# Optimization experiments

Hardware: AMD Instinct MI355X
Metric: run time of the kernel (lower is better)

## Reference

```python
import jax, jax.numpy as jnp
import numpy as np

H = 16
D_MODEL = 1024
HEAD_DIM = D_MODEL // H
NEG = -1e9


def setup_inputs() -> dict:
    key = jax.random.key(0)
    k1, k2, k3, k4, k5, k6 = jax.random.split(key, 6)
    B, L = 2, 2048
    feature = jax.random.normal(k1, (B, L, D_MODEL), dtype=jnp.float32)
    mask = jax.random.randint(k2, (B, L), 0, 2, dtype=jnp.int32)
    # Linear weights stored torch-style as [out, in]; biases zero-init per initialize().
    s = 1.0 / np.sqrt(D_MODEL)
    W_Q = jax.random.uniform(k3, (D_MODEL, D_MODEL), jnp.float32, -s, s)
    W_K = jax.random.uniform(k4, (D_MODEL, D_MODEL), jnp.float32, -s, s)
    W_V = jax.random.uniform(k5, (D_MODEL, D_MODEL), jnp.float32, -s, s)
    b_Q = jnp.zeros((D_MODEL,), jnp.float32)
    b_K = jnp.zeros((D_MODEL,), jnp.float32)
    b_V = jnp.zeros((D_MODEL,), jnp.float32)
    return {"feature": feature, "mask": mask, "W_Q": W_Q, "b_Q": b_Q,
            "W_K": W_K, "b_K": b_K, "W_V": W_V, "b_V": b_V}


def reference(feature, mask, W_Q, b_Q, W_K, b_K, W_V, b_V):
    B, L, _ = feature.shape
    scale = jnp.sqrt(jnp.float32(HEAD_DIM))
    # Projections: torch Linear is x @ W^T + b. Split into heads: [B, H, L, Dh]
    def proj(W, b):
        y = feature @ W.T + b
        return y.reshape(B, L, H, HEAD_DIM).transpose(0, 2, 1, 3)
    Q = proj(W_Q, b_Q)
    K = proj(W_K, b_K)
    V = proj(W_V, b_V)
    # Scores [B, H, Lq, Lk]
    A = jnp.einsum('bhqd,bhkd->bhqk', Q, K) / scale
    # Key-side mask broadcast over heads and query positions
    A = jnp.where(mask[:, None, None, :] == 0, jnp.float32(NEG), A)
    alpha = jax.nn.softmax(A, axis=-1)
    out = jnp.einsum('bhqk,bhkd->bhqd', alpha, V)  # [B, H, L, Dh]
    return out.transpose(0, 2, 1, 3).reshape(B, L, H * HEAD_DIM)
```

## Files before the change

kernel.cpp:

```cpp
#include <hip/hip_runtime.h>

typedef __bf16 bf16;
typedef __attribute__((ext_vector_type(8))) __bf16 bf16x8;
typedef __attribute__((ext_vector_type(4))) float f32x4;
typedef __attribute__((ext_vector_type(16))) float f32x16;
typedef unsigned int u32;

#define D_MODEL 1024
#define SEQ_L   2048
#define NHEAD   16
#define HDIM    64
#define MROWS   4096

#define FEAT_OFF  512u
#define WQ_OFF    (FEAT_OFF + 4194304u)
#define WK_OFF    (WQ_OFF + 1048576u)
#define WV_OFF    (WK_OFF + 1048576u)
#define BQ_OFF    (WV_OFF + 1048576u)
#define BK_OFF    (BQ_OFF + 1024u)
#define BV_OFF    (BK_OFF + 1024u)
#define Q_OFF     (BV_OFF + 1024u)
#define K_OFF     (Q_OFF + 4194304u)
#define V_OFF     (K_OFF + 4194304u)

__device__ __forceinline__ bf16 f2bf(float f) {
    unsigned u = __builtin_bit_cast(unsigned, f);
    unsigned r = (u + 0x7fffu + ((u >> 16) & 1u)) >> 16;
    unsigned short s = (unsigned short)r;
    return __builtin_bit_cast(bf16, s);
}

typedef const __attribute__((address_space(1))) u32* gp_t;
typedef __attribute__((address_space(3))) u32* lp_t;
__device__ __forceinline__ void ld16(const bf16* g, bf16* l) {
    __builtin_amdgcn_global_load_lds((gp_t)g, (lp_t)l, 16, 0, 0);
}

__global__ void convert_in(const float* __restrict__ feat,
                           const float* __restrict__ wq, const float* __restrict__ wk,
                           const float* __restrict__ wv,
                           const float* __restrict__ bq, const float* __restrict__ bk,
                           const float* __restrict__ bv,
                           bf16* __restrict__ ws) {
    const float* src; bf16* dst; int n;
    switch (blockIdx.y) {
        case 0: src = feat; dst = ws + FEAT_OFF; n = 4194304; break;
        case 1: src = wq;   dst = ws + WQ_OFF;   n = 1048576; break;
        case 2: src = wk;   dst = ws + WK_OFF;   n = 1048576; break;
        case 3: src = wv;   dst = ws + WV_OFF;   n = 1048576; break;
        case 4: src = bq;   dst = ws + BQ_OFF;   n = 1024;    break;
        case 5: src = bk;   dst = ws + BK_OFF;   n = 1024;    break;
        default: src = bv;  dst = ws + BV_OFF;   n = 1024;    break;
    }
    int idx = (blockIdx.x * 256 + threadIdx.x) * 4;
    if (idx >= n) return;
    float4 v = ((const float4*)src)[idx >> 2];
    dst[idx + 0] = f2bf(v.x);
    dst[idx + 1] = f2bf(v.y);
    dst[idx + 2] = f2bf(v.z);
    dst[idx + 3] = f2bf(v.w);
}

__global__ __launch_bounds__(256, 2) void qkv_gemm(const bf16* __restrict__ ws,
                                                   bf16* __restrict__ wsw) {
    const int zi = blockIdx.z;
    const bf16* Amat = (zi == 2) ? ws + WV_OFF : ws + FEAT_OFF;
    const bf16* Bmat = (zi == 0) ? ws + WQ_OFF : (zi == 1) ? ws + WK_OFF : ws + FEAT_OFF;
    const bf16* bias = ws + ((zi == 0) ? BQ_OFF : (zi == 1) ? BK_OFF : BV_OFF);
    bf16* Y = (zi == 2) ? wsw + V_OFF : wsw + Q_OFF + (size_t)zi * 4194304u;

    __shared__ bf16 Alds[128 * 64];
    __shared__ bf16 Blds[128 * 64];

    const int t    = threadIdx.x;
    const int lane = t & 63;
    const int wave = t >> 6;
    const int quad = lane >> 4;
    const int l16  = lane & 15;
    const int m0   = ((zi == 2) ? blockIdx.y : blockIdx.x) * 128;
    const int n0   = ((zi == 2) ? blockIdx.x : blockIdx.y) * 128;
    const int wrow = (wave >> 1) * 64;
    const int wcol = (wave & 1) * 64;

    const int r8 = lane >> 3;
    const int sl = lane & 7;
    const int sg = sl ^ r8;

    f32x4 acc[4][4];
    for (int mi = 0; mi < 4; ++mi)
        for (int ni = 0; ni < 4; ++ni)
            acc[mi][ni] = (f32x4){0.f, 0.f, 0.f, 0.f};

    for (int k0 = 0; k0 < D_MODEL; k0 += 64) {
#pragma unroll
        for (int i = 0; i < 4; ++i) {
            int ch  = wave * 4 + i;
            int row = ch * 8 + r8;
            ld16(Amat + (size_t)(m0 + row) * D_MODEL + k0 + sg * 8, Alds + ch * 512);
            ld16(Bmat + (size_t)(n0 + row) * D_MODEL + k0 + sg * 8, Blds + ch * 512);
        }
        __syncthreads();

#pragma unroll
        for (int kk = 0; kk < 2; ++kk) {
            const int sgb = quad + kk * 4;
            bf16x8 af[4], bfr[4];
#pragma unroll
            for (int mi = 0; mi < 4; ++mi) {
                int row = wrow + mi * 16 + l16;
                af[mi] = *(const bf16x8*)(&Alds[row * 64 + ((sgb ^ (row & 7)) << 3)]);
            }
#pragma unroll
            for (int ni = 0; ni < 4; ++ni) {
                int row = wcol + ni * 16 + l16;
                bfr[ni] = *(const bf16x8*)(&Blds[row * 64 + ((sgb ^ (row & 7)) << 3)]);
            }
#pragma unroll
            for (int mi = 0; mi < 4; ++mi)
#pragma unroll
                for (int ni = 0; ni < 4; ++ni)
                    acc[mi][ni] = __builtin_amdgcn_mfma_f32_16x16x32_bf16(
                        af[mi], bfr[ni], acc[mi][ni], 0, 0, 0);
        }
        __syncthreads();
    }

    if (zi < 2) {
#pragma unroll
        for (int ni = 0; ni < 4; ++ni) {
            int col = n0 + wcol + ni * 16 + l16;
            float bvf = (float)bias[col];
#pragma unroll
            for (int mi = 0; mi < 4; ++mi) {
                int rowb = m0 + wrow + mi * 16 + quad * 4;
#pragma unroll
                for (int r = 0; r < 4; ++r)
                    Y[(size_t)(rowb + r) * D_MODEL + col] = f2bf(acc[mi][ni][r] + bvf);
            }
        }
    } else {
#pragma unroll
        for (int mi = 0; mi < 4; ++mi) {
#pragma unroll
            for (int r = 0; r < 4; ++r) {
                int rowv = m0 + wrow + mi * 16 + quad * 4 + r;
                float bvf = (float)bias[rowv];
#pragma unroll
                for (int ni = 0; ni < 4; ++ni) {
                    int col = n0 + wcol + ni * 16 + l16;
                    size_t addr = (size_t)(col >> 11) * 2097152u +
                                  (size_t)rowv * 2048u + (col & 2047);
                    Y[addr] = f2bf(acc[mi][ni][r] + bvf);
                }
            }
        }
    }
}

#define KSTR 68
#define PSTR 68

__global__ __launch_bounds__(128, 2) void attn_kernel(
    const bf16* __restrict__ ws, const int* __restrict__ mask,
    float* __restrict__ out) {
    const int qt = blockIdx.x;
    const int bh = blockIdx.y;
    const int b  = bh >> 4, h = bh & 15;
    const int t    = threadIdx.x;
    const int lane = t & 63;
    const int wave = t >> 6;
    const int half = lane >> 5;
    const int l32  = lane & 31;

    __shared__ bf16 Klds[64 * KSTR];
    __shared__ bf16 Vlds[64 * KSTR];
    __shared__ bf16 Plds[2][32 * PSTR];
    __shared__ float mlds[64];

    const bf16* Qh  = ws + Q_OFF + (size_t)(b * SEQ_L) * D_MODEL + h * HDIM;
    const bf16* Kh  = ws + K_OFF + (size_t)(b * SEQ_L) * D_MODEL + h * HDIM;
    const bf16* Vth = ws + V_OFF + (size_t)b * 2097152u + (size_t)(h * HDIM) * SEQ_L;

    const int qrow = qt * 64 + wave * 32 + l32;
    bf16x8 qf[4];
#pragma unroll
    for (int ks = 0; ks < 4; ++ks) {
        qf[ks] = *(const bf16x8*)(Qh + (size_t)qrow * D_MODEL + ks * 16 + half * 8);
#pragma unroll
        for (int j = 0; j < 8; ++j)
            qf[ks][j] = (bf16)((float)qf[ks][j] * 0.125f);
    }

    f32x16 o0, o1;
    float lsum[16];
#pragma unroll
    for (int i = 0; i < 16; ++i) { o0[i] = 0.f; o1[i] = 0.f; lsum[i] = 0.f; }

    for (int kt = 0; kt < SEQ_L; kt += 64) {
#pragma unroll
        for (int i = 0; i < 4; ++i) {
            int c = t + 128 * i;
            int row = c >> 3, seg = c & 7;
            uint4 kv = *(const uint4*)(Kh + (size_t)(kt + row) * D_MODEL + seg * 8);
            *(uint4*)(&Klds[row * KSTR + seg * 8]) = kv;
            uint4 vv = *(const uint4*)(Vth + (size_t)row * SEQ_L + kt + seg * 8);
            *(uint4*)(&Vlds[row * KSTR + seg * 8]) = vv;
        }
        if (t < 64) mlds[t] = (mask[b * SEQ_L + kt + t] != 0) ? 0.f : -1e9f;
        __syncthreads();

        f32x16 s0, s1;
#pragma unroll
        for (int i = 0; i < 16; ++i) { s0[i] = 0.f; s1[i] = 0.f; }
#pragma unroll
        for (int ks = 0; ks < 4; ++ks) {
            bf16x8 kf0 = *(const bf16x8*)(&Klds[l32 * KSTR + ks * 16 + half * 8]);
            bf16x8 kf1 = *(const bf16x8*)(&Klds[(32 + l32) * KSTR + ks * 16 + half * 8]);
            s0 = __builtin_amdgcn_mfma_f32_32x32x16_bf16(qf[ks], kf0, s0, 0, 0, 0);
            s1 = __builtin_amdgcn_mfma_f32_32x32x16_bf16(qf[ks], kf1, s1, 0, 0, 0);
        }

        const float mb0 = mlds[l32];
        const float mb1 = mlds[32 + l32];
#pragma unroll
        for (int reg = 0; reg < 16; ++reg) {
            int row = (reg & 3) + 8 * (reg >> 2) + 4 * half;
            float p0 = __expf(s0[reg] + mb0);
            float p1 = __expf(s1[reg] + mb1);
            lsum[reg] += p0 + p1;
            Plds[wave][row * PSTR + l32]      = (bf16)p0;
            Plds[wave][row * PSTR + 32 + l32] = (bf16)p1;
        }

#pragma unroll
        for (int ks = 0; ks < 4; ++ks) {
            bf16x8 pf  = *(const bf16x8*)(&Plds[wave][l32 * PSTR + ks * 16 + half * 8]);
            bf16x8 vf0 = *(const bf16x8*)(&Vlds[l32 * KSTR + ks * 16 + half * 8]);
            bf16x8 vf1 = *(const bf16x8*)(&Vlds[(32 + l32) * KSTR + ks * 16 + half * 8]);
            o0 = __builtin_amdgcn_mfma_f32_32x32x16_bf16(pf, vf0, o0, 0, 0, 0);
            o1 = __builtin_amdgcn_mfma_f32_32x32x16_bf16(pf, vf1, o1, 0, 0, 0);
        }
        __syncthreads();
    }

#pragma unroll
    for (int reg = 0; reg < 16; ++reg) {
#pragma unroll
        for (int off = 1; off < 32; off <<= 1)
            lsum[reg] += __shfl_xor(lsum[reg], off);
        lsum[reg] = 1.0f / fmaxf(lsum[reg], 1e-30f);
    }

#pragma unroll
    for (int reg = 0; reg < 16; ++reg) {
        int row = (reg & 3) + 8 * (reg >> 2) + 4 * half;
        int q = qt * 64 + wave * 32 + row;
        size_t base = ((size_t)(b * SEQ_L + q)) * D_MODEL + h * HDIM;
        out[base + l32]      = o0[reg] * lsum[reg];
        out[base + 32 + l32] = o1[reg] * lsum[reg];
    }
}

extern "C" void kernel_launch(void* const* d_in, const int* in_sizes, int n_in,
                              void* d_out, int out_size, void* d_ws, size_t ws_size,
                              hipStream_t stream) {
    const float* feat = (const float*)d_in[0];
    const int*   mask = (const int*)d_in[1];
    const float* Wq = (const float*)d_in[2];
    const float* bq = (const float*)d_in[3];
    const float* Wk = (const float*)d_in[4];
    const float* bk = (const float*)d_in[5];
    const float* Wv = (const float*)d_in[6];
    const float* bv = (const float*)d_in[7];

    bf16* ws = (bf16*)d_ws;

    dim3 gc(4096, 7);
    convert_in<<<gc, 256, 0, stream>>>(feat, Wq, Wk, Wv, bq, bk, bv, ws);

    dim3 g1(32, 8, 3);
    qkv_gemm<<<g1, 256, 0, stream>>>(ws, ws);

    dim3 g2(SEQ_L / 64, 2 * NHEAD);
    attn_kernel<<<g2, 128, 0, stream>>>(ws, mask, (float*)d_out);
}
```

Baseline: 192.8 us.

## Enlarge attention query tile, prefetch K/V into registers, transpose score MFMA

Each attention wave now handles 64 query rows (two 32-row sub-tiles) instead of 32, so every K/V tile loaded to LDS is reused across twice as many queries, and the grid is halved. The next K/V tile and mask are prefetched into registers while the current tile is computed. Scores are computed as K·Q^T so each lane holds one query's scores, which reduces the row-sum to a single cross-half shuffle and gives packed bf16x4 P stores. The mask becomes a ballot bitmask applied after exp, and launch bounds change for both kernels, trading higher register pressure and lower occupancy for more data reuse.

```diff
diff --git a/kernel.cpp b/kernel.cpp
--- a/kernel.cpp
+++ b/kernel.cpp
@@ -1,6 +1,7 @@
 #include <hip/hip_runtime.h>
 
 typedef __bf16 bf16;
+typedef __attribute__((ext_vector_type(4))) __bf16 bf16x4;
 typedef __attribute__((ext_vector_type(8))) __bf16 bf16x8;
 typedef __attribute__((ext_vector_type(4))) float f32x4;
 typedef __attribute__((ext_vector_type(16))) float f32x16;
@@ -61,7 +62,7 @@
     dst[idx + 3] = f2bf(v.w);
 }
 
-__global__ __launch_bounds__(256, 2) void qkv_gemm(const bf16* __restrict__ ws,
+__global__ __launch_bounds__(256, 3) void qkv_gemm(const bf16* __restrict__ ws,
                                                    bf16* __restrict__ wsw) {
     const int zi = blockIdx.z;
     const bf16* Amat = (zi == 2) ? ws + WV_OFF : ws + FEAT_OFF;
@@ -160,7 +161,7 @@
 #define KSTR 68
 #define PSTR 68
 
-__global__ __launch_bounds__(128, 2) void attn_kernel(
+__global__ __launch_bounds__(128, 1) void attn_kernel(
     const bf16* __restrict__ ws, const int* __restrict__ mask,
     float* __restrict__ out) {
     const int qt = blockIdx.x;
@@ -170,94 +171,161 @@
     const int lane = t & 63;
     const int wave = t >> 6;
     const int half = lane >> 5;
-    const int l32  = lane & 31;
+    const int l31  = lane & 31;
 
     __shared__ bf16 Klds[64 * KSTR];
     __shared__ bf16 Vlds[64 * KSTR];
-    __shared__ bf16 Plds[2][32 * PSTR];
-    __shared__ float mlds[64];
+    __shared__ bf16 Plds[2][64 * PSTR];
 
     const bf16* Qh  = ws + Q_OFF + (size_t)(b * SEQ_L) * D_MODEL + h * HDIM;
     const bf16* Kh  = ws + K_OFF + (size_t)(b * SEQ_L) * D_MODEL + h * HDIM;
     const bf16* Vth = ws + V_OFF + (size_t)b * 2097152u + (size_t)(h * HDIM) * SEQ_L;
 
-    const int qrow = qt * 64 + wave * 32 + l32;
-    bf16x8 qf[4];
-#pragma unroll
-    for (int ks = 0; ks < 4; ++ks) {
-        qf[ks] = *(const bf16x8*)(Qh + (size_t)qrow * D_MODEL + ks * 16 + half * 8);
-#pragma unroll
-        for (int j = 0; j < 8; ++j)
-            qf[ks][j] = (bf16)((float)qf[ks][j] * 0.125f);
-    }
-
-    f32x16 o0, o1;
-    float lsum[16];
-#pragma unroll
-    for (int i = 0; i < 16; ++i) { o0[i] = 0.f; o1[i] = 0.f; lsum[i] = 0.f; }
+    const int qbase = qt * 128 + wave * 64;
+    bf16x8 qf[2][4];
+#pragma unroll
+    for (int qs = 0; qs < 2; ++qs)
+#pragma unroll
+        for (int ks = 0; ks < 4; ++ks) {
+            qf[qs][ks] = *(const bf16x8*)(Qh + (size_t)(qbase + qs * 32 + l31) * D_MODEL
+                                          + ks * 16 + half * 8);
+#pragma unroll
+            for (int j = 0; j < 8; ++j)
+                qf[qs][ks][j] = (bf16)((float)qf[qs][ks][j] * 0.125f);
+        }
+
+    f32x16 o[2][2];
+    float lsum[2] = {0.f, 0.f};
+#pragma unroll
+    for (int qs = 0; qs < 2; ++qs)
+#pragma unroll
+        for (int dt = 0; dt < 2; ++dt)
+#pragma unroll
+            for (int i = 0; i < 16; ++i) o[qs][dt][i] = 0.f;
+
+    uint4 kr[4], vr[4];
+    int mv;
+    {
+        const int row0 = t >> 3, seg0 = t & 7;
+#pragma unroll
+        for (int i = 0; i < 4; ++i) {
+            int row = row0 + 16 * i;
+            kr[i] = *(const uint4*)(Kh + (size_t)row * D_MODEL + seg0 * 8);
+            vr[i] = *(const uint4*)(Vth + (size_t)row * SEQ_L + seg0 * 8);
+        }
+        mv = mask[b * SEQ_L + lane];
+    }
 
     for (int kt = 0; kt < SEQ_L; kt += 64) {
+        const int row0 = t >> 3, seg0 = t & 7;
 #pragma unroll
         for (int i = 0; i < 4; ++i) {
-            int c = t + 128 * i;
-            int row = c >> 3, seg = c & 7;
-            uint4 kv = *(const uint4*)(Kh + (size_t)(kt + row) * D_MODEL + seg * 8);
-            *(uint4*)(&Klds[row * KSTR + seg * 8]) = kv;
-            uint4 vv = *(const uint4*)(Vth + (size_t)row * SEQ_L + kt + seg * 8);
-            *(uint4*)(&Vlds[row * KSTR + seg * 8]) = vv;
-        }
-        if (t < 64) mlds[t] = (mask[b * SEQ_L + kt + t] != 0) ? 0.f : -1e9f;
+            int row = row0 + 16 * i;
+            *(uint4*)(&Klds[row * KSTR + seg0 * 8]) = kr[i];
+            *(uint4*)(&Vlds[row * KSTR + seg0 * 8]) = vr[i];
+        }
+        unsigned long long bm = __ballot(mv != 0);
+        const unsigned m0s = ((unsigned)bm) >> (half * 4);
+        const unsigned m1s = ((unsigned)(bm >> 32)) >> (half * 4);
         __syncthreads();
 
-        f32x16 s0, s1;
-#pragma unroll
-        for (int i = 0; i < 16; ++i) { s0[i] = 0.f; s1[i] = 0.f; }
-#pragma unroll
-        for (int ks = 0; ks < 4; ++ks) {
-            bf16x8 kf0 = *(const bf16x8*)(&Klds[l32 * KSTR + ks * 16 + half * 8]);
-            bf16x8 kf1 = *(const bf16x8*)(&Klds[(32 + l32) * KSTR + ks * 16 + half * 8]);
-            s0 = __builtin_amdgcn_mfma_f32_32x32x16_bf16(qf[ks], kf0, s0, 0, 0, 0);
-            s1 = __builtin_amdgcn_mfma_f32_32x32x16_bf16(qf[ks], kf1, s1, 0, 0, 0);
-        }
-
-        const float mb0 = mlds[l32];
-        const float mb1 = mlds[32 + l32];
-#pragma unroll
-        for (int reg = 0; reg < 16; ++reg) {
-            int row = (reg & 3) + 8 * (reg >> 2) + 4 * half;
-            float p0 = __expf(s0[reg] + mb0);
-            float p1 = __expf(s1[reg] + mb1);
-            lsum[reg] += p0 + p1;
-            Plds[wave][row * PSTR + l32]      = (bf16)p0;
-            Plds[wave][row * PSTR + 32 + l32] = (bf16)p1;
-        }
-
-#pragma unroll
-        for (int ks = 0; ks < 4; ++ks) {
-            bf16x8 pf  = *(const bf16x8*)(&Plds[wave][l32 * PSTR + ks * 16 + half * 8]);
-            bf16x8 vf0 = *(const bf16x8*)(&Vlds[l32 * KSTR + ks * 16 + half * 8]);
-            bf16x8 vf1 = *(const bf16x8*)(&Vlds[(32 + l32) * KSTR + ks * 16 + half * 8]);
-            o0 = __builtin_amdgcn_mfma_f32_32x32x16_bf16(pf, vf0, o0, 0, 0, 0);
-            o1 = __builtin_amdgcn_mfma_f32_32x32x16_bf16(pf, vf1, o1, 0, 0, 0);
-        }
+        if (kt + 64 < SEQ_L) {
+#pragma unroll
+            for (int i = 0; i < 4; ++i) {
+                int row = row0 + 16 * i;
+                kr[i] = *(const uint4*)(Kh + (size_t)(kt + 64 + row) * D_MODEL + seg0 * 8);
+                vr[i] = *(const uint4*)(Vth + (size_t)row * SEQ_L + kt + 64 + seg0 * 8);
+            }
+            mv = mask[b * SEQ_L + kt + 64 + lane];
+        }
+
+        bf16x8 kf[2][4];
+#pragma unroll
+        for (int ktile = 0; ktile < 2; ++ktile)
+#pragma unroll
+            for (int ks = 0; ks < 4; ++ks)
+                kf[ktile][ks] = *(const bf16x8*)(&Klds[(ktile * 32 + l31) * KSTR
+                                                       + ks * 16 + half * 8]);
+        f32x16 st[2][2];
+#pragma unroll
+        for (int qs = 0; qs < 2; ++qs)
+#pragma unroll
+            for (int ktile = 0; ktile < 2; ++ktile) {
+#pragma unroll
+                for (int i = 0; i < 16; ++i) st[qs][ktile][i] = 0.f;
+#pragma unroll
+                for (int ks = 0; ks < 4; ++ks)
+                    st[qs][ktile] = __builtin_amdgcn_mfma_f32_32x32x16_bf16(
+                        kf[ktile][ks], qf[qs][ks], st[qs][ktile], 0, 0, 0);
+            }
+
+#pragma unroll
+        for (int qs = 0; qs < 2; ++qs) {
+            const int prow = (qs * 32 + l31) * PSTR;
+#pragma unroll
+            for (int ktile = 0; ktile < 2; ++ktile) {
+                const unsigned ms = ktile ? m1s : m0s;
+                float pp[16];
+#pragma unroll
+                for (int r = 0; r < 16; ++r) {
+                    const int kb = (r & 3) + 8 * (r >> 2);
+                    float p = __expf(st[qs][ktile][r]);
+                    p = ((ms >> kb) & 1u) ? p : 0.f;
+                    lsum[qs] += p;
+                    pp[r] = p;
+                }
+#pragma unroll
+                for (int g = 0; g < 4; ++g) {
+                    bf16x4 pk;
+#pragma unroll
+                    for (int j = 0; j < 4; ++j) pk[j] = f2bf(pp[g * 4 + j]);
+                    *(bf16x4*)(&Plds[wave][prow + ktile * 32 + g * 8 + half * 4]) = pk;
+                }
+            }
+        }
+
+        bf16x8 pf[2][4], vf[2][4];
+#pragma unroll
+        for (int qs = 0; qs < 2; ++qs)
+#pragma unroll
+            for (int ks = 0; ks < 4; ++ks)
+                pf[qs][ks] = *(const bf16x8*)(&Plds[wave][(qs * 32 + l31) * PSTR
+                                                          + ks * 16 + half * 8]);
+#pragma unroll
+        for (int dt = 0; dt < 2; ++dt)
+#pragma unroll
+            for (int ks = 0; ks < 4; ++ks)
+                vf[dt][ks] = *(const bf16x8*)(&Vlds[(dt * 32 + l31) * KSTR
+                                                    + ks * 16 + half * 8]);
+#pragma unroll
+        for (int qs = 0; qs < 2; ++qs)
+#pragma unroll
+            for (int dt = 0; dt < 2; ++dt)
+#pragma unroll
+                for (int ks = 0; ks < 4; ++ks)
+                    o[qs][dt] = __builtin_amdgcn_mfma_f32_32x32x16_bf16(
+                        pf[qs][ks], vf[dt][ks], o[qs][dt], 0, 0, 0);
         __syncthreads();
     }
 
-#pragma unroll
-    for (int reg = 0; reg < 16; ++reg) {
-#pragma unroll
-        for (int off = 1; off < 32; off <<= 1)
-            lsum[reg] += __shfl_xor(lsum[reg], off);
-        lsum[reg] = 1.0f / fmaxf(lsum[reg], 1e-30f);
-    }
-
-#pragma unroll
-    for (int reg = 0; reg < 16; ++reg) {
-        int row = (reg & 3) + 8 * (reg >> 2) + 4 * half;
-        int q = qt * 64 + wave * 32 + row;
-        size_t base = ((size_t)(b * SEQ_L + q)) * D_MODEL + h * HDIM;
-        out[base + l32]      = o0[reg] * lsum[reg];
-        out[base + 32 + l32] = o1[reg] * lsum[reg];
+    float inv[2];
+#pragma unroll
+    for (int qs = 0; qs < 2; ++qs) {
+        float l = lsum[qs] + __shfl_xor(lsum[qs], 32);
+        inv[qs] = 1.0f / fmaxf(l, 1e-30f);
+    }
+
+#pragma unroll
+    for (int qs = 0; qs < 2; ++qs) {
+#pragma unroll
+        for (int r = 0; r < 16; ++r) {
+            const int q32 = (r & 3) + 8 * (r >> 2) + 4 * half;
+            const float rl = __shfl(inv[qs], q32);
+            const int q = qbase + qs * 32 + q32;
+            const size_t base = ((size_t)(b * SEQ_L + q)) * D_MODEL + h * HDIM;
+            out[base + l31]      = o[qs][0][r] * rl;
+            out[base + 32 + l31] = o[qs][1][r] * rl;
+        }
     }
 }
 
@@ -281,6 +349,6 @@
     dim3 g1(32, 8, 3);
     qkv_gemm<<<g1, 256, 0, stream>>>(ws, ws);
 
-    dim3 g2(SEQ_L / 64, 2 * NHEAD);
+    dim3 g2(SEQ_L / 128, 2 * NHEAD);
     attn_kernel<<<g2, 128, 0, stream>>>(ws, mask, (float*)d_out);
 }
```

New measurement: 236.6 us. 1.23x slower.
